# Kernel tuning notes

Hardware: AMD Instinct MI355X
Metric: run time of the kernel (lower is better)

Reference implementation:

```python
import jax, jax.numpy as jnp
import numpy as np

B, S, D_IN, H, D_HEAD = 8, 1024, 768, 12, 64

def setup_inputs() -> dict:
    key = jax.random.key(0)
    k1, k2, k3, k4 = jax.random.split(key, 4)
    x = jax.random.normal(k1, (B, S, D_IN), dtype=jnp.float32)
    # per-head projection weights, stacked: [H, d_in, d_head]
    scale = 1.0 / np.sqrt(D_IN)
    Wq = jax.random.normal(k2, (H, D_IN, D_HEAD), dtype=jnp.float32) * scale
    Wk = jax.random.normal(k3, (H, D_IN, D_HEAD), dtype=jnp.float32) * scale
    Wv = jax.random.normal(k4, (H, D_IN, D_HEAD), dtype=jnp.float32) * scale
    return {"x": x, "Wq": Wq, "Wk": Wk, "Wv": Wv}

def reference(x, Wq, Wk, Wv) -> jnp.ndarray:
    # Batched equivalent of the Python loop over heads + concat.
    q = jnp.einsum('bsd,hde->bhse', x, Wq)  # [B,H,S,Dh]
    k = jnp.einsum('bsd,hde->bhse', x, Wk)
    v = jnp.einsum('bsd,hde->bhse', x, Wv)
    scores = jnp.einsum('bhse,bhte->bhst', q, k) / jnp.sqrt(jnp.asarray(D_HEAD, x.dtype))
    causal = jnp.tril(jnp.ones((S, S), dtype=bool))  # [S,S]
    scores = jnp.where(causal, scores, jnp.asarray(-jnp.inf, x.dtype))
    attn = jax.nn.softmax(scores, axis=-1)  # dropout p=0.0 -> identity
    ctx = jnp.einsum('bhst,bhte->bhse', attn, v)  # [B,H,S,Dh]
    # concat heads along last dim -> [B,S,H*Dh]
    return jnp.transpose(ctx, (0, 2, 1, 3)).reshape(B, S, H * D_HEAD)
```

## Files before the change

kernel.cpp:

```cpp
#include <hip/hip_runtime.h>

typedef short short8 __attribute__((ext_vector_type(8)));
typedef float f32x4 __attribute__((ext_vector_type(4)));
typedef float f32x16 __attribute__((ext_vector_type(16)));

#define SQ   1024
#define DIN  768
#define NH   12
#define DH   64
#define SCL2 0.1803368801111243f

static __device__ __forceinline__ ushort f2bf(float f) {
  union { float f; unsigned u; } v; v.f = f;
  unsigned u = v.u;
  unsigned r = (u + 0x7FFFu + ((u >> 16) & 1u)) >> 16;
  return (ushort)r;
}
static __device__ __forceinline__ unsigned pk2(float a, float b) {
  return (unsigned)f2bf(a) | ((unsigned)f2bf(b) << 16);
}

static __device__ __forceinline__ void gload_lds16(const ushort* g, ushort* l) {
  __builtin_amdgcn_global_load_lds(
      (const __attribute__((address_space(1))) unsigned*)(g),
      (__attribute__((address_space(3))) unsigned*)(l),
      16, 0, 0);
}

__global__ __launch_bounds__(256) void k_convert_x(const float* __restrict__ x,
                                                   ushort* __restrict__ xb) {
  int i = (blockIdx.x * 256 + threadIdx.x) * 4;
  float4 v = *reinterpret_cast<const float4*>(x + i);
  ushort4 o;
  o.x = f2bf(v.x); o.y = f2bf(v.y); o.z = f2bf(v.z); o.w = f2bf(v.w);
  *reinterpret_cast<ushort4*>(xb + i) = o;
}

__global__ __launch_bounds__(256) void k_prep_w(const float* __restrict__ Wq,
                                                const float* __restrict__ Wk,
                                                const float* __restrict__ Wv,
                                                ushort* __restrict__ wt) {
  __shared__ ushort tile[64][65];
  const int mh = blockIdx.x;
  const int m = mh / 12, h = mh % 12;
  const int d0 = blockIdx.y * 64;
  const float* W = (m == 0 ? Wq : (m == 1 ? Wk : Wv)) + h * DIN * DH;
  ushort* outp = wt + (size_t)mh * DH * DIN;
  #pragma unroll
  for (int p = 0; p < 16; ++p) {
    int idx = p * 256 + threadIdx.x;
    int d = idx >> 6, e = idx & 63;
    tile[d][e] = f2bf(W[(d0 + d) * DH + e]);
  }
  __syncthreads();
  #pragma unroll
  for (int p = 0; p < 16; ++p) {
    int idx = p * 256 + threadIdx.x;
    int e = idx >> 6, d = idx & 63;
    outp[e * DIN + d0 + d] = tile[d][e];
  }
}

__global__ __launch_bounds__(256) void k_proj(const ushort* __restrict__ xb,
                                              const ushort* __restrict__ wt,
                                              ushort* __restrict__ qo,
                                              ushort* __restrict__ ko,
                                              ushort* __restrict__ vto) {
  __shared__ __align__(16) ushort Sb[16384];

  const int brow = blockIdx.x * 128;
  const int bn   = blockIdx.y * 128;
  const int w    = threadIdx.x >> 6, lane = threadIdx.x & 63;
  const int lr   = lane & 15, lg = lane >> 4;
  const int wm   = w >> 1, wn = w & 1;

  const int srow  = threadIdx.x >> 2;
  const int sslot = (threadIdx.x & 3) ^ (srow & 3) ^ ((srow >> 2) & 3);
  const ushort* gA = xb + (size_t)(brow + srow) * DIN + sslot * 8;
  const ushort* gB = wt + (size_t)(bn   + srow) * DIN + sslot * 8;

  f32x4 acc[4][4];
  #pragma unroll
  for (int i = 0; i < 4; ++i)
    #pragma unroll
    for (int j = 0; j < 4; ++j) acc[i][j] = (f32x4){0.f, 0.f, 0.f, 0.f};

  const int fr   = (lr & 3) ^ ((lr >> 2) & 3);
  const int aoff = (lg ^ fr) * 8;

#define STAGEP(bi, tt) do {                                               \
    const int k0_ = (tt) * 32;                                            \
    ushort* la_ = Sb + (bi) * 4096 + threadIdx.x * 8;                     \
    ushort* lb_ = Sb + 8192 + (bi) * 4096 + threadIdx.x * 8;              \
    gload_lds16(gA + k0_,            la_);                                \
    gload_lds16(gA + k0_ + 64 * DIN, la_ + 2048);                         \
    gload_lds16(gB + k0_,            lb_);                                \
    gload_lds16(gB + k0_ + 64 * DIN, lb_ + 2048);                         \
  } while (0)

  STAGEP(0, 0);
  __syncthreads();

  int cur = 0;
  #pragma unroll 1
  for (int t = 0; t < 24; ++t) {
    if (t + 1 < 24) STAGEP(cur ^ 1, t + 1);
    short8 a[4], b[4];
    #pragma unroll
    for (int mi = 0; mi < 4; ++mi)
      a[mi] = *reinterpret_cast<const short8*>(&Sb[cur * 4096 + (wm * 64 + mi * 16 + lr) * 32 + aoff]);
    #pragma unroll
    for (int ci = 0; ci < 4; ++ci)
      b[ci] = *reinterpret_cast<const short8*>(&Sb[8192 + cur * 4096 + (wn * 64 + ci * 16 + lr) * 32 + aoff]);
    #pragma unroll
    for (int mi = 0; mi < 4; ++mi)
      #pragma unroll
      for (int ci = 0; ci < 4; ++ci)
        acc[mi][ci] = __builtin_amdgcn_mfma_f32_16x16x32_bf16(a[mi], b[ci], acc[mi][ci], 0, 0, 0);
    __syncthreads();
    cur ^= 1;
  }
#undef STAGEP

  ushort* ldsw = Sb + w * 4096;
  const int colbase = bn + wn * 64;
  const int mh = colbase >> 6;
  const int m = mh / 12, h = mh % 12;
  const int c = lane & 7;

  if (m < 2) {
    #pragma unroll
    for (int mi = 0; mi < 4; ++mi)
      #pragma unroll
      for (int ci = 0; ci < 4; ++ci)
        #pragma unroll
        for (int r = 0; r < 4; ++r) {
          int sl = mi * 16 + lg * 4 + r;
          int e  = ci * 16 + lr;
          ldsw[sl * 64 + (e ^ ((sl & 7) << 3))] = f2bf(acc[mi][ci][r]);
        }
    asm volatile("s_waitcnt lgkmcnt(0)" ::: "memory");
    ushort* dst = (m == 0) ? qo : ko;
    #pragma unroll
    for (int it = 0; it < 8; ++it) {
      int sl = it * 8 + (lane >> 3);
      short8 vv = *reinterpret_cast<const short8*>(&ldsw[sl * 64 + ((c * 8) ^ ((sl & 7) << 3))]);
      int rg = brow + wm * 64 + sl;
      int b_ = rg >> 10, s_ = rg & 1023;
      *reinterpret_cast<short8*>(dst + ((size_t)(b_ * 12 + h) * SQ + s_) * DH + c * 8) = vv;
    }
  } else {
    #pragma unroll
    for (int mi = 0; mi < 4; ++mi)
      #pragma unroll
      for (int ci = 0; ci < 4; ++ci)
        #pragma unroll
        for (int r = 0; r < 4; ++r) {
          int sl = mi * 16 + lg * 4 + r;
          int e  = ci * 16 + lr;
          ldsw[e * 64 + (sl ^ ((e & 7) << 3))] = f2bf(acc[mi][ci][r]);
        }
    asm volatile("s_waitcnt lgkmcnt(0)" ::: "memory");
    #pragma unroll
    for (int it = 0; it < 8; ++it) {
      int e = it * 8 + (lane >> 3);
      short8 vv = *reinterpret_cast<const short8*>(&ldsw[e * 64 + ((c * 8) ^ ((e & 7) << 3))]);
      int rg = brow + wm * 64 + c * 8;
      int b_ = rg >> 10, s_ = rg & 1023;
      *reinterpret_cast<short8*>(vto + ((size_t)(b_ * 12 + h) * DH + e) * SQ + s_) = vv;
    }
  }
}

__global__ __launch_bounds__(256, 3) void k_attn(const ushort* __restrict__ qi,
                                                 const ushort* __restrict__ ki,
                                                 const ushort* __restrict__ vti,
                                                 float* __restrict__ out) {
  __shared__ __align__(16) ushort Kb[2][64 * 64];
  __shared__ __align__(16) ushort Vb[2][64 * 64];

  const int f = blockIdx.x;
  const int g = f >> 8, r_ = f & 255;
  const int qt = ((r_ & 7) + g * 3) & 7;
  const int bh = g * 32 + (r_ >> 3);
  const int b = bh / 12, h = bh % 12;
  const int w = threadIdx.x >> 6, lane = threadIdx.x & 63;
  const int ql = lane & 31, hi = lane >> 5;
  const int q0 = qt * 128 + w * 32;
  const int nt = (q0 >> 6) + 1;
  const int ntmax = 2 * qt + 2;
  const ushort* qb = qi  + (size_t)bh * SQ * DH;
  const ushort* kb = ki  + (size_t)bh * SQ * DH;
  const ushort* vb = vti + (size_t)bh * DH * SQ;

  short8 qf[4];
  #pragma unroll
  for (int m = 0; m < 4; ++m)
    qf[m] = *reinterpret_cast<const short8*>(qb + (size_t)(q0 + ql) * DH + m * 16 + hi * 8);

  f32x16 o0, o1;
  #pragma unroll
  for (int r = 0; r < 16; ++r) { o0[r] = 0.f; o1[r] = 0.f; }
  float m_run = -1e30f, l_run = 0.f;

#define STAGE(bufi, tt) do {                                                                   \
    const int kv0_ = (tt) * 64;                                                                \
    const int t0 = threadIdx.x, t1 = threadIdx.x + 256;                                        \
    gload_lds16(kb + (size_t)(kv0_ + (t0 >> 3)) * DH + (((t0 & 7) ^ ((t0 >> 3) & 7)) * 8),     \
                &Kb[bufi][0] + t0 * 8);                                                        \
    gload_lds16(kb + (size_t)(kv0_ + (t1 >> 3)) * DH + (((t1 & 7) ^ ((t1 >> 3) & 7)) * 8),     \
                &Kb[bufi][0] + t1 * 8);                                                        \
    gload_lds16(vb + (size_t)(t0 >> 3) * SQ + kv0_ + (((t0 & 7) ^ ((t0 >> 3) & 7)) * 8),       \
                &Vb[bufi][0] + t0 * 8);                                                        \
    gload_lds16(vb + (size_t)(t1 >> 3) * SQ + kv0_ + (((t1 & 7) ^ ((t1 >> 3) & 7)) * 8),       \
                &Vb[bufi][0] + t1 * 8);                                                        \
  } while (0)

  STAGE(0, 0);
  __syncthreads();

  int cur = 0;
  #pragma unroll 1
  for (int t = 0; t < ntmax; ++t) {
    if (t + 1 < ntmax) STAGE(cur ^ 1, t + 1);

    if (t < nt) {
      const int kv0 = t * 64;
      const ushort* Kc = &Kb[cur][0];
      const ushort* Vc = &Vb[cur][0];

      f32x16 s0, s1;
      #pragma unroll
      for (int r = 0; r < 16; ++r) { s0[r] = 0.f; s1[r] = 0.f; }
      #pragma unroll
      for (int m = 0; m < 4; ++m) {
        short8 kf = *reinterpret_cast<const short8*>(Kc + ql * 64 + ((2 * m + hi) ^ (ql & 7)) * 8);
        s0 = __builtin_amdgcn_mfma_f32_32x32x16_bf16(kf, qf[m], s0, 0, 0, 0);
      }
      #pragma unroll
      for (int m = 0; m < 4; ++m) {
        short8 kf = *reinterpret_cast<const short8*>(Kc + (32 + ql) * 64 + ((2 * m + hi) ^ (ql & 7)) * 8);
        s1 = __builtin_amdgcn_mfma_f32_32x32x16_bf16(kf, qf[m], s1, 0, 0, 0);
      }

      if (t == nt - 1) {
        const int qg = q0 + ql;
        #pragma unroll
        for (int r = 0; r < 16; ++r) {
          int kvl = (r & 3) + 8 * (r >> 2) + 4 * hi;
          if (kv0 + kvl      > qg) s0[r] = -1e30f;
          if (kv0 + 32 + kvl > qg) s1[r] = -1e30f;
        }
      }

      float mt = s0[0];
      #pragma unroll
      for (int r = 1; r < 16; ++r) mt = fmaxf(mt, s0[r]);
      #pragma unroll
      for (int r = 0; r < 16; ++r) mt = fmaxf(mt, s1[r]);
      mt = fmaxf(mt, __shfl_xor(mt, 32));
      if (__any(mt > m_run + 40.0f)) {
        float mnew = fmaxf(m_run, mt);
        float corr = exp2f((m_run - mnew) * SCL2);
        l_run *= corr; m_run = mnew;
        #pragma unroll
        for (int r = 0; r < 16; ++r) {
          float cr = __shfl(corr, (r & 3) + 8 * (r >> 2) + 4 * hi);
          o0[r] *= cr; o1[r] *= cr;
        }
      }
      float ts = 0.f;
      #pragma unroll
      for (int r = 0; r < 16; ++r) {
        s0[r] = exp2f((s0[r] - m_run) * SCL2); ts += s0[r];
        s1[r] = exp2f((s1[r] - m_run) * SCL2); ts += s1[r];
      }
      ts += __shfl_xor(ts, 32);
      l_run += ts;

#define PV_CHUNK(SV, CC, KC) do {                                                              \
        unsigned wa = pk2(SV[(CC) * 8 + 0], SV[(CC) * 8 + 1]);                                 \
        unsigned wb = pk2(SV[(CC) * 8 + 2], SV[(CC) * 8 + 3]);                                 \
        unsigned wc = pk2(SV[(CC) * 8 + 4], SV[(CC) * 8 + 5]);                                 \
        unsigned wd = pk2(SV[(CC) * 8 + 6], SV[(CC) * 8 + 7]);                                 \
        unsigned xa = __shfl_xor(wa, 32), xb2 = __shfl_xor(wb, 32);                            \
        unsigned xc = __shfl_xor(wc, 32), xd = __shfl_xor(wd, 32);                             \
        uint4 pw;                                                                              \
        pw.x = hi ? xc : wa;  pw.y = hi ? xd : wb;                                             \
        pw.z = hi ? wc : xa;  pw.w = hi ? wd : xb2;                                            \
        short8 pa = *reinterpret_cast<short8*>(&pw);                                           \
        short8 vf0 = *reinterpret_cast<const short8*>(Vc + ql * 64 +                           \
                       ((2 * (KC) + hi) ^ (ql & 7)) * 8);                                      \
        o0 = __builtin_amdgcn_mfma_f32_32x32x16_bf16(pa, vf0, o0, 0, 0, 0);                    \
        short8 vf1 = *reinterpret_cast<const short8*>(Vc + (32 + ql) * 64 +                    \
                       ((2 * (KC) + hi) ^ (ql & 7)) * 8);                                      \
        o1 = __builtin_amdgcn_mfma_f32_32x32x16_bf16(pa, vf1, o1, 0, 0, 0);                    \
      } while (0)

      PV_CHUNK(s0, 0, 0);
      PV_CHUNK(s0, 1, 1);
      PV_CHUNK(s1, 0, 2);
      PV_CHUNK(s1, 1, 3);
#undef PV_CHUNK
    }

    __syncthreads();
    cur ^= 1;
  }
#undef STAGE

  float rl = 1.0f / l_run;
  #pragma unroll
  for (int r = 0; r < 16; ++r) {
    int base = (r & 3) + 8 * (r >> 2) + 4 * hi;
    float sc_ = __shfl(rl, base);
    int qg = q0 + base;
    float* op = out + ((size_t)b * SQ + qg) * (NH * DH) + h * DH;
    op[ql]      = o0[r] * sc_;
    op[32 + ql] = o1[r] * sc_;
  }
}

extern "C" void kernel_launch(void* const* d_in, const int* in_sizes, int n_in,
                              void* d_out, int out_size, void* d_ws, size_t ws_size,
                              hipStream_t stream) {
  const float* x  = (const float*)d_in[0];
  const float* Wq = (const float*)d_in[1];
  const float* Wk = (const float*)d_in[2];
  const float* Wv = (const float*)d_in[3];
  float* out = (float*)d_out;

  char* ws = (char*)d_ws;
  ushort* xb = (ushort*)(ws);
  ushort* wt = (ushort*)(ws + 12582912);
  ushort* q  = (ushort*)(ws + 16121856);
  ushort* k  = (ushort*)(ws + 28704768);
  ushort* vt = (ushort*)(ws + 41287680);

  k_convert_x<<<6144, 256, 0, stream>>>(x, xb);
  k_prep_w<<<dim3(36, 12), 256, 0, stream>>>(Wq, Wk, Wv, wt);
  k_proj<<<dim3(64, 18), 256, 0, stream>>>(xb, wt, q, k, vt);
  k_attn<<<768, 256, 0, stream>>>(q, k, vt, out);
}
```

Measured before the change: 177.7 us.

## Enlarge projection GEMM tile and use hardware packed bf16 conversion

```diff
diff --git a/kernel.cpp b/kernel.cpp
--- a/kernel.cpp
+++ b/kernel.cpp
@@ -16,8 +16,10 @@
   unsigned r = (u + 0x7FFFu + ((u >> 16) & 1u)) >> 16;
   return (ushort)r;
 }
-static __device__ __forceinline__ unsigned pk2(float a, float b) {
-  return (unsigned)f2bf(a) | ((unsigned)f2bf(b) << 16);
+static __device__ __forceinline__ unsigned cvtpk(float a, float b) {
+  unsigned r;
+  asm("v_cvt_pk_bf16_f32 %0, %1, %2" : "=v"(r) : "v"(a), "v"(b));
+  return r;
 }
 
 static __device__ __forceinline__ void gload_lds16(const ushort* g, ushort* l) {
@@ -29,11 +31,13 @@
 
 __global__ __launch_bounds__(256) void k_convert_x(const float* __restrict__ x,
                                                    ushort* __restrict__ xb) {
-  int i = (blockIdx.x * 256 + threadIdx.x) * 4;
-  float4 v = *reinterpret_cast<const float4*>(x + i);
-  ushort4 o;
-  o.x = f2bf(v.x); o.y = f2bf(v.y); o.z = f2bf(v.z); o.w = f2bf(v.w);
-  *reinterpret_cast<ushort4*>(xb + i) = o;
+  int i = (blockIdx.x * 256 + threadIdx.x) * 8;
+  float4 v0 = *reinterpret_cast<const float4*>(x + i);
+  float4 v1 = *reinterpret_cast<const float4*>(x + i + 4);
+  uint4 o;
+  o.x = cvtpk(v0.x, v0.y); o.y = cvtpk(v0.z, v0.w);
+  o.z = cvtpk(v1.x, v1.y); o.w = cvtpk(v1.z, v1.w);
+  *reinterpret_cast<uint4*>(xb + i) = o;
 }
 
 __global__ __launch_bounds__(256) void k_prep_w(const float* __restrict__ Wq,
@@ -61,14 +65,14 @@
   }
 }
 
-__global__ __launch_bounds__(256) void k_proj(const ushort* __restrict__ xb,
-                                              const ushort* __restrict__ wt,
-                                              ushort* __restrict__ qo,
-                                              ushort* __restrict__ ko,
-                                              ushort* __restrict__ vto) {
-  __shared__ __align__(16) ushort Sb[16384];
-
-  const int brow = blockIdx.x * 128;
+__global__ __launch_bounds__(256, 2) void k_proj(const ushort* __restrict__ xb,
+                                                 const ushort* __restrict__ wt,
+                                                 ushort* __restrict__ qo,
+                                                 ushort* __restrict__ ko,
+                                                 ushort* __restrict__ vto) {
+  __shared__ __align__(16) ushort Sb[24576];
+
+  const int brow = blockIdx.x * 256;
   const int bn   = blockIdx.y * 128;
   const int w    = threadIdx.x >> 6, lane = threadIdx.x & 63;
   const int lr   = lane & 15, lg = lane >> 4;
@@ -79,9 +83,9 @@
   const ushort* gA = xb + (size_t)(brow + srow) * DIN + sslot * 8;
   const ushort* gB = wt + (size_t)(bn   + srow) * DIN + sslot * 8;
 
-  f32x4 acc[4][4];
-  #pragma unroll
-  for (int i = 0; i < 4; ++i)
+  f32x4 acc[8][4];
+  #pragma unroll
+  for (int i = 0; i < 8; ++i)
     #pragma unroll
     for (int j = 0; j < 4; ++j) acc[i][j] = (f32x4){0.f, 0.f, 0.f, 0.f};
 
@@ -90,12 +94,14 @@
 
 #define STAGEP(bi, tt) do {                                               \
     const int k0_ = (tt) * 32;                                            \
-    ushort* la_ = Sb + (bi) * 4096 + threadIdx.x * 8;                     \
-    ushort* lb_ = Sb + 8192 + (bi) * 4096 + threadIdx.x * 8;              \
-    gload_lds16(gA + k0_,            la_);                                \
-    gload_lds16(gA + k0_ + 64 * DIN, la_ + 2048);                         \
-    gload_lds16(gB + k0_,            lb_);                                \
-    gload_lds16(gB + k0_ + 64 * DIN, lb_ + 2048);                         \
+    ushort* la_ = Sb + (bi) * 8192 + threadIdx.x * 8;                     \
+    ushort* lb_ = Sb + 16384 + (bi) * 4096 + threadIdx.x * 8;             \
+    gload_lds16(gA + k0_,             la_);                               \
+    gload_lds16(gA + k0_ +  64 * DIN, la_ + 2048);                        \
+    gload_lds16(gA + k0_ + 128 * DIN, la_ + 4096);                        \
+    gload_lds16(gA + k0_ + 192 * DIN, la_ + 6144);                        \
+    gload_lds16(gB + k0_,             lb_);                               \
+    gload_lds16(gB + k0_ +  64 * DIN, lb_ + 2048);                        \
   } while (0)
 
   STAGEP(0, 0);
@@ -105,15 +111,15 @@
   #pragma unroll 1
   for (int t = 0; t < 24; ++t) {
     if (t + 1 < 24) STAGEP(cur ^ 1, t + 1);
-    short8 a[4], b[4];
+    short8 a[8], b[4];
     #pragma unroll
-    for (int mi = 0; mi < 4; ++mi)
-      a[mi] = *reinterpret_cast<const short8*>(&Sb[cur * 4096 + (wm * 64 + mi * 16 + lr) * 32 + aoff]);
+    for (int mi = 0; mi < 8; ++mi)
+      a[mi] = *reinterpret_cast<const short8*>(&Sb[cur * 8192 + (wm * 128 + mi * 16 + lr) * 32 + aoff]);
     #pragma unroll
     for (int ci = 0; ci < 4; ++ci)
-      b[ci] = *reinterpret_cast<const short8*>(&Sb[8192 + cur * 4096 + (wn * 64 + ci * 16 + lr) * 32 + aoff]);
+      b[ci] = *reinterpret_cast<const short8*>(&Sb[16384 + cur * 4096 + (wn * 64 + ci * 16 + lr) * 32 + aoff]);
     #pragma unroll
-    for (int mi = 0; mi < 4; ++mi)
+    for (int mi = 0; mi < 8; ++mi)
       #pragma unroll
       for (int ci = 0; ci < 4; ++ci)
         acc[mi][ci] = __builtin_amdgcn_mfma_f32_16x16x32_bf16(a[mi], b[ci], acc[mi][ci], 0, 0, 0);
@@ -123,51 +129,53 @@
 #undef STAGEP
 
   ushort* ldsw = Sb + w * 4096;
-  const int colbase = bn + wn * 64;
-  const int mh = colbase >> 6;
+  const int mh = blockIdx.y * 2 + wn;
   const int m = mh / 12, h = mh % 12;
   const int c = lane & 7;
 
-  if (m < 2) {
-    #pragma unroll
-    for (int mi = 0; mi < 4; ++mi)
-      #pragma unroll
-      for (int ci = 0; ci < 4; ++ci)
+  #pragma unroll
+  for (int p = 0; p < 2; ++p) {
+    if (m < 2) {
+      #pragma unroll
+      for (int mi2 = 0; mi2 < 4; ++mi2)
         #pragma unroll
-        for (int r = 0; r < 4; ++r) {
-          int sl = mi * 16 + lg * 4 + r;
-          int e  = ci * 16 + lr;
-          ldsw[sl * 64 + (e ^ ((sl & 7) << 3))] = f2bf(acc[mi][ci][r]);
-        }
-    asm volatile("s_waitcnt lgkmcnt(0)" ::: "memory");
-    ushort* dst = (m == 0) ? qo : ko;
-    #pragma unroll
-    for (int it = 0; it < 8; ++it) {
-      int sl = it * 8 + (lane >> 3);
-      short8 vv = *reinterpret_cast<const short8*>(&ldsw[sl * 64 + ((c * 8) ^ ((sl & 7) << 3))]);
-      int rg = brow + wm * 64 + sl;
-      int b_ = rg >> 10, s_ = rg & 1023;
-      *reinterpret_cast<short8*>(dst + ((size_t)(b_ * 12 + h) * SQ + s_) * DH + c * 8) = vv;
-    }
-  } else {
-    #pragma unroll
-    for (int mi = 0; mi < 4; ++mi)
-      #pragma unroll
-      for (int ci = 0; ci < 4; ++ci)
+        for (int ci = 0; ci < 4; ++ci)
+          #pragma unroll
+          for (int r = 0; r < 4; ++r) {
+            int sl = mi2 * 16 + lg * 4 + r;
+            int e  = ci * 16 + lr;
+            ldsw[sl * 64 + (e ^ ((sl & 7) << 3))] = f2bf(acc[p * 4 + mi2][ci][r]);
+          }
+      asm volatile("s_waitcnt lgkmcnt(0)" ::: "memory");
+      ushort* dst = (m == 0) ? qo : ko;
+      #pragma unroll
+      for (int it = 0; it < 8; ++it) {
+        int sl = it * 8 + (lane >> 3);
+        short8 vv = *reinterpret_cast<const short8*>(&ldsw[sl * 64 + ((c * 8) ^ ((sl & 7) << 3))]);
+        int rg = brow + wm * 128 + p * 64 + sl;
+        int b_ = rg >> 10, s_ = rg & 1023;
+        *reinterpret_cast<short8*>(dst + ((size_t)(b_ * 12 + h) * SQ + s_) * DH + c * 8) = vv;
+      }
+    } else {
+      #pragma unroll
+      for (int mi2 = 0; mi2 < 4; ++mi2)
         #pragma unroll
-        for (int r = 0; r < 4; ++r) {
-          int sl = mi * 16 + lg * 4 + r;
-          int e  = ci * 16 + lr;
-          ldsw[e * 64 + (sl ^ ((e & 7) << 3))] = f2bf(acc[mi][ci][r]);
-        }
-    asm volatile("s_waitcnt lgkmcnt(0)" ::: "memory");
-    #pragma unroll
-    for (int it = 0; it < 8; ++it) {
-      int e = it * 8 + (lane >> 3);
-      short8 vv = *reinterpret_cast<const short8*>(&ldsw[e * 64 + ((c * 8) ^ ((e & 7) << 3))]);
-      int rg = brow + wm * 64 + c * 8;
-      int b_ = rg >> 10, s_ = rg & 1023;
-      *reinterpret_cast<short8*>(vto + ((size_t)(b_ * 12 + h) * DH + e) * SQ + s_) = vv;
+        for (int ci = 0; ci < 4; ++ci)
+          #pragma unroll
+          for (int r = 0; r < 4; ++r) {
+            int sl = mi2 * 16 + lg * 4 + r;
+            int e  = ci * 16 + lr;
+            ldsw[e * 64 + (sl ^ ((e & 7) << 3))] = f2bf(acc[p * 4 + mi2][ci][r]);
+          }
+      asm volatile("s_waitcnt lgkmcnt(0)" ::: "memory");
+      #pragma unroll
+      for (int it = 0; it < 8; ++it) {
+        int e = it * 8 + (lane >> 3);
+        short8 vv = *reinterpret_cast<const short8*>(&ldsw[e * 64 + ((c * 8) ^ ((e & 7) << 3))]);
+        int rg = brow + wm * 128 + p * 64 + c * 8;
+        int b_ = rg >> 10, s_ = rg & 1023;
+        *reinterpret_cast<short8*>(vto + ((size_t)(b_ * 12 + h) * DH + e) * SQ + s_) = vv;
+      }
     }
   }
 }
@@ -279,10 +287,10 @@
       l_run += ts;
 
 #define PV_CHUNK(SV, CC, KC) do {                                                              \
-        unsigned wa = pk2(SV[(CC) * 8 + 0], SV[(CC) * 8 + 1]);                                 \
-        unsigned wb = pk2(SV[(CC) * 8 + 2], SV[(CC) * 8 + 3]);                                 \
-        unsigned wc = pk2(SV[(CC) * 8 + 4], SV[(CC) * 8 + 5]);                                 \
-        unsigned wd = pk2(SV[(CC) * 8 + 6], SV[(CC) * 8 + 7]);                                 \
+        unsigned wa = cvtpk(SV[(CC) * 8 + 0], SV[(CC) * 8 + 1]);                               \
+        unsigned wb = cvtpk(SV[(CC) * 8 + 2], SV[(CC) * 8 + 3]);                               \
+        unsigned wc = cvtpk(SV[(CC) * 8 + 4], SV[(CC) * 8 + 5]);                               \
+        unsigned wd = cvtpk(SV[(CC) * 8 + 6], SV[(CC) * 8 + 7]);                               \
         unsigned xa = __shfl_xor(wa, 32), xb2 = __shfl_xor(wb, 32);                            \
         unsigned xc = __shfl_xor(wc, 32), xd = __shfl_xor(wd, 32);                             \
         uint4 pw;                                                                              \
@@ -337,8 +345,8 @@
   ushort* k  = (ushort*)(ws + 28704768);
   ushort* vt = (ushort*)(ws + 41287680);
 
-  k_convert_x<<<6144, 256, 0, stream>>>(x, xb);
+  k_convert_x<<<3072, 256, 0, stream>>>(x, xb);
   k_prep_w<<<dim3(36, 12), 256, 0, stream>>>(Wq, Wk, Wv, wt);
-  k_proj<<<dim3(64, 18), 256, 0, stream>>>(xb, wt, q, k, vt);
+  k_proj<<<dim3(32, 18), 256, 0, stream>>>(xb, wt, q, k, vt);
   k_attn<<<768, 256, 0, stream>>>(q, k, vt, out);
 }
```

Result: faster. 171.3 us (-3.6%).
